# Kernel optimization log

Hardware: AMD Instinct MI355X
Metric: run time of the kernel (lower is better)

## Reference

```python
import jax, jax.numpy as jnp
import numpy as np

B, T, I, H, TGT = 256, 4096, 8, 32, 8


def setup_inputs() -> dict:
    key = jax.random.key(0)
    ks = jax.random.split(key, 6)
    return {
        "inputs": jax.random.normal(ks[0], (B, T, I), jnp.float32),
        "encode_weights": jax.random.normal(ks[1], (H, I), jnp.float32) * 0.3,   # xavier-ish
        "w_ih": jax.random.normal(ks[2], (3 * H, H), jnp.float32) * 0.1,        # GRU weight_ih_l0
        "w_hh": jax.random.normal(ks[3], (3 * H, H), jnp.float32) * 0.1,        # GRU weight_hh_l0
        "b_ih": jax.random.normal(ks[4], (3 * H,), jnp.float32) * 0.1,
        "b_hh": jax.random.normal(ks[5], (3 * H,), jnp.float32) * 0.1,
    }


def _gru(gx_t, w_hh, b_hh, h0):
    # gx_t: time-major input-gate pre-activations [T, B, 3H]; PyTorch GRU math:
    # r = sig(gx_r + gh_r); z = sig(gx_z + gh_z); n = tanh(gx_n + r*gh_n); h = (1-z)*n + z*h
    Hd = h0.shape[-1]
    def step(h, gx):
        gh = h @ w_hh.T + b_hh                      # [B, 3H]
        r = jax.nn.sigmoid(gx[..., :Hd] + gh[..., :Hd])
        z = jax.nn.sigmoid(gx[..., Hd:2 * Hd] + gh[..., Hd:2 * Hd])
        n = jnp.tanh(gx[..., 2 * Hd:] + r * gh[..., 2 * Hd:])
        h_new = (1.0 - z) * n + z * h
        return h_new, h_new
    _, hs = jax.lax.scan(step, h0, gx_t)            # hs: [T, B, H]
    return hs


def reference(inputs, encode_weights, w_ih, w_hh, b_ih, b_hh):
    # encode = F.linear(inputs, encode_weights)
    encode = jnp.einsum('bti,hi->bth', inputs, encode_weights)      # [B, T, H]
    gx = jnp.einsum('bth,gh->btg', encode, w_ih) + b_ih             # [B, T, 3H]
    gx_t = jnp.swapaxes(gx, 0, 1)                                   # [T, B, 3H]
    h0 = jnp.zeros((inputs.shape[0], encode_weights.shape[0]), inputs.dtype)
    latents = jnp.swapaxes(_gru(gx_t, w_hh, b_hh, h0), 0, 1)        # [B, T, H]
    # tied decoder: F.linear(latents, encode_weights[:, :target_size].T)
    outputs = jnp.einsum('bth,ho->bto', latents, encode_weights[:, :TGT])
    return outputs, latents
```

## Files before the change

### kernel.cpp

```cpp
#include <hip/hip_runtime.h>
#include <hip/hip_bf16.h>
#include <cstdint>
#include <cstddef>

#define Bsz  256
#define Tn   4096
#define In   8
#define Hn   32
#define Gn   96
#define TGTn 8
#define CH   256

__device__ __forceinline__ float rcpf(float x) { return __builtin_amdgcn_rcpf(x); }
__device__ __forceinline__ float sigm(float x) { return rcpf(1.f + __expf(-x)); }
__device__ __forceinline__ float tanhfast(float x) {
    float e = __expf(2.f * x);
    return 1.f - 2.f * rcpf(e + 1.f);
}

__global__ void fuse_wih_kernel(const float* __restrict__ w_ih,
                                const float* __restrict__ E,
                                float* __restrict__ Wf) {
    int tid = threadIdx.x;
    int g = tid >> 3, i = tid & 7;
    float acc = 0.f;
#pragma unroll
    for (int k = 0; k < Hn; ++k)
        acc = fmaf(w_ih[g * Hn + k], E[k * In + i], acc);
    Wf[g * In + i] = acc;
}

__launch_bounds__(64, 1)
__global__ void gru_kernel(const float* __restrict__ x,
                           const float* __restrict__ Wf,
                           const float* __restrict__ w_hh,
                           const float* __restrict__ b_ih,
                           const float* __restrict__ b_hh,
                           float* __restrict__ latents) {
    __shared__ __align__(16) float lds_h[Hn];
    __shared__ __align__(16) float lds_x[CH * In];
    __shared__ __align__(16) float lds_lat[CH * Hn];

    const int lane = threadIdx.x;
    const int grp  = lane >> 5;
    const int j    = lane & 31;
    const int b    = blockIdx.x;

    const float* xb  = x + (size_t)b * Tn * In;
    float* latb      = latents + (size_t)b * Tn * Hn;

    float whr[16], whz[16], whn[16];
#pragma unroll
    for (int q = 0; q < 4; ++q) {
        float4 vr = *(const float4*)&w_hh[(0 * Hn + j) * Hn + grp * 16 + q * 4];
        float4 vz = *(const float4*)&w_hh[(1 * Hn + j) * Hn + grp * 16 + q * 4];
        float4 vn = *(const float4*)&w_hh[(2 * Hn + j) * Hn + grp * 16 + q * 4];
        whr[q*4+0] = vr.x; whr[q*4+1] = vr.y; whr[q*4+2] = vr.z; whr[q*4+3] = vr.w;
        whz[q*4+0] = vz.x; whz[q*4+1] = vz.y; whz[q*4+2] = vz.z; whz[q*4+3] = vz.w;
        whn[q*4+0] = vn.x; whn[q*4+1] = vn.y; whn[q*4+2] = vn.z; whn[q*4+3] = vn.w;
    }
    const float4 wxr = *(const float4*)&Wf[(0 * Hn + j) * In + grp * 4];
    const float4 wxz = *(const float4*)&Wf[(1 * Hn + j) * In + grp * 4];
    const float4 wxn = *(const float4*)&Wf[(2 * Hn + j) * In + grp * 4];

    const float br  = b_ih[j]          + b_hh[j];
    const float bz  = b_ih[Hn + j]     + b_hh[Hn + j];
    const float bxn = b_ih[2 * Hn + j];
    const float bhn = b_hh[2 * Hn + j];

    float hj = 0.f;
    float h16[16];
#pragma unroll
    for (int q = 0; q < 16; ++q) h16[q] = 0.f;

    for (int t0 = 0; t0 < Tn; t0 += CH) {
#pragma unroll
        for (int c = 0; c < 8; ++c) {
            int f4 = c * 64 + lane;
            float4 v = *(const float4*)&xb[(size_t)t0 * In + (size_t)f4 * 4];
            *(float4*)&lds_x[f4 * 4] = v;
        }
        __syncthreads();

#pragma unroll 1
        for (int s = 0; s < CH; ++s) {
            float4 xv = *(const float4*)&lds_x[s * In + grp * 4];

            float ar0 = 0.f, ar1 = 0.f, az0 = 0.f, az1 = 0.f, an0 = 0.f, an1 = 0.f;
#pragma unroll
            for (int q = 0; q < 8; ++q) {
                ar0 = fmaf(h16[2*q],   whr[2*q],   ar0);
                ar1 = fmaf(h16[2*q+1], whr[2*q+1], ar1);
                az0 = fmaf(h16[2*q],   whz[2*q],   az0);
                az1 = fmaf(h16[2*q+1], whz[2*q+1], az1);
                an0 = fmaf(h16[2*q],   whn[2*q],   an0);
                an1 = fmaf(h16[2*q+1], whn[2*q+1], an1);
            }
            float ar   = ar0 + ar1;
            float az   = az0 + az1;
            float aghn = an0 + an1;
            ar = fmaf(xv.x, wxr.x, ar); ar = fmaf(xv.y, wxr.y, ar);
            ar = fmaf(xv.z, wxr.z, ar); ar = fmaf(xv.w, wxr.w, ar);
            az = fmaf(xv.x, wxz.x, az); az = fmaf(xv.y, wxz.y, az);
            az = fmaf(xv.z, wxz.z, az); az = fmaf(xv.w, wxz.w, az);
            float agxn = xv.x * wxn.x;
            agxn = fmaf(xv.y, wxn.y, agxn);
            agxn = fmaf(xv.z, wxn.z, agxn);
            agxn = fmaf(xv.w, wxn.w, agxn);

            ar   += __shfl_xor(ar, 32);
            az   += __shfl_xor(az, 32);
            aghn += __shfl_xor(aghn, 32);
            agxn += __shfl_xor(agxn, 32);

            float r = sigm(ar + br);
            float z = sigm(az + bz);
            float n = tanhfast(agxn + bxn + r * (aghn + bhn));
            hj = n + z * (hj - n);

            __syncthreads();
            if (grp == 0) {
                lds_h[j] = hj;
                lds_lat[s * Hn + j] = hj;
            }
            __syncthreads();
#pragma unroll
            for (int q = 0; q < 4; ++q) {
                float4 hv = *(const float4*)&lds_h[grp * 16 + q * 4];
                h16[q*4+0] = hv.x; h16[q*4+1] = hv.y;
                h16[q*4+2] = hv.z; h16[q*4+3] = hv.w;
            }
        }
        __syncthreads();
#pragma unroll
        for (int c = 0; c < 32; ++c) {
            int f4 = c * 64 + lane;
            float4 v = *(const float4*)&lds_lat[f4 * 4];
            *(float4*)&latb[(size_t)t0 * Hn + (size_t)f4 * 4] = v;
        }
    }
}

__global__ void decode_kernel(const float* __restrict__ lat,
                              const float* __restrict__ E,
                              float* __restrict__ out) {
    __shared__ float ldsE[Hn * TGTn];
    int tid = threadIdx.x;
    if (tid < Hn * TGTn) ldsE[tid] = E[tid];
    __syncthreads();
    size_t idx = (size_t)blockIdx.x * 256 + tid;
    int o      = (int)(idx & (TGTn - 1));
    size_t row = idx >> 3;
    const float* lrow = lat + row * Hn;
    float acc = 0.f;
#pragma unroll
    for (int h = 0; h < Hn; ++h)
        acc = fmaf(lrow[h], ldsE[h * TGTn + o], acc);
    out[idx] = acc;
}

extern "C" void kernel_launch(void* const* d_in, const int* in_sizes, int n_in,
                              void* d_out, int out_size, void* d_ws, size_t ws_size,
                              hipStream_t stream) {
    const float* x    = (const float*)d_in[0];
    const float* E    = (const float*)d_in[1];
    const float* w_ih = (const float*)d_in[2];
    const float* w_hh = (const float*)d_in[3];
    const float* b_ih = (const float*)d_in[4];
    const float* b_hh = (const float*)d_in[5];

    float* out = (float*)d_out;
    float* lat = out + (size_t)Bsz * Tn * TGTn;
    float* Wf  = (float*)d_ws;

    fuse_wih_kernel<<<1, 768, 0, stream>>>(w_ih, E, Wf);
    gru_kernel<<<Bsz, 64, 0, stream>>>(x, Wf, w_hh, b_ih, b_hh, lat);
    decode_kernel<<<(Bsz * Tn * TGTn) / 256, 256, 0, stream>>>(lat, E, out);
}
```

Baseline: 1.156 ms.

## Replace LDS hidden-state exchange with DPP/permlane cross-lane gathers and packed FMAs

The recurrent loop no longer passes the hidden state through shared memory with two barriers per step. Each lane now rebuilds its half of h in registers using permlane16/32 swaps and DPP row rotates, with w_hh columns pre-permuted to match the rotated order. The half-wave reductions use permlane32_swap, the matvec uses packed v2f FMAs, and inputs stream through an 8-deep register ring instead of LDS staging. Latents are written straight to global memory each step rather than buffered, which trades coalesced bulk stores for per-step 128-byte stores.

```diff
diff --git a/kernel.cpp b/kernel.cpp
--- a/kernel.cpp
+++ b/kernel.cpp
@@ -7,9 +7,45 @@
 #define Tn   4096
 #define In   8
 #define Hn   32
-#define Gn   96
 #define TGTn 8
-#define CH   256
+
+typedef float v2f __attribute__((ext_vector_type(2)));
+
+__device__ __forceinline__ v2f pk_fma(v2f a, v2f b, v2f c) {
+    return __builtin_elementwise_fma(a, b, c);
+}
+
+template<int N>
+__device__ __forceinline__ float dpp_ror(float x) {
+    int xi = __float_as_int(x);
+    int r = __builtin_amdgcn_update_dpp(xi, xi, 0x120 + N, 0xF, 0xF, false);
+    return __int_as_float(r);
+}
+
+__device__ __forceinline__ float half_sum(float x) {
+    auto r = __builtin_amdgcn_permlane32_swap(__float_as_int(x), __float_as_int(x),
+                                              false, false);
+    return __int_as_float((int)r[0]) + __int_as_float((int)r[1]);
+}
+
+__device__ __forceinline__ void row16_pair(float x, float& a_out, float& b_out) {
+    auto r = __builtin_amdgcn_permlane16_swap(__float_as_int(x), __float_as_int(x),
+                                              false, false);
+    a_out = __int_as_float((int)r[0]);
+    b_out = __int_as_float((int)r[1]);
+}
+
+__device__ __forceinline__ void gather16(float v, v2f H[8]) {
+    v2f G0; G0.x = v;                G0.y = dpp_ror<1>(v);
+    v2f G1; G1.x = dpp_ror<2>(G0.x); G1.y = dpp_ror<2>(G0.y);
+    v2f G2; G2.x = dpp_ror<4>(G0.x); G2.y = dpp_ror<4>(G0.y);
+    v2f G3; G3.x = dpp_ror<4>(G1.x); G3.y = dpp_ror<4>(G1.y);
+    v2f G4; G4.x = dpp_ror<8>(G0.x); G4.y = dpp_ror<8>(G0.y);
+    v2f G5; G5.x = dpp_ror<8>(G1.x); G5.y = dpp_ror<8>(G1.y);
+    v2f G6; G6.x = dpp_ror<8>(G2.x); G6.y = dpp_ror<8>(G2.y);
+    v2f G7; G7.x = dpp_ror<8>(G3.x); G7.y = dpp_ror<8>(G3.y);
+    H[0]=G0; H[1]=G1; H[2]=G2; H[3]=G3; H[4]=G4; H[5]=G5; H[6]=G6; H[7]=G7;
+}
 
 __device__ __forceinline__ float rcpf(float x) { return __builtin_amdgcn_rcpf(x); }
 __device__ __forceinline__ float sigm(float x) { return rcpf(1.f + __expf(-x)); }
@@ -37,106 +73,121 @@
                            const float* __restrict__ b_ih,
                            const float* __restrict__ b_hh,
                            float* __restrict__ latents) {
-    __shared__ __align__(16) float lds_h[Hn];
-    __shared__ __align__(16) float lds_x[CH * In];
-    __shared__ __align__(16) float lds_lat[CH * Hn];
-
-    const int lane = threadIdx.x;
+    const int lane = threadIdx.x & 63;
     const int grp  = lane >> 5;
     const int j    = lane & 31;
+    const int r16  = lane & 15;
     const int b    = blockIdx.x;
 
-    const float* xb  = x + (size_t)b * Tn * In;
-    float* latb      = latents + (size_t)b * Tn * Hn;
-
-    float whr[16], whz[16], whn[16];
-#pragma unroll
-    for (int q = 0; q < 4; ++q) {
-        float4 vr = *(const float4*)&w_hh[(0 * Hn + j) * Hn + grp * 16 + q * 4];
-        float4 vz = *(const float4*)&w_hh[(1 * Hn + j) * Hn + grp * 16 + q * 4];
-        float4 vn = *(const float4*)&w_hh[(2 * Hn + j) * Hn + grp * 16 + q * 4];
-        whr[q*4+0] = vr.x; whr[q*4+1] = vr.y; whr[q*4+2] = vr.z; whr[q*4+3] = vr.w;
-        whz[q*4+0] = vz.x; whz[q*4+1] = vz.y; whz[q*4+2] = vz.z; whz[q*4+3] = vz.w;
-        whn[q*4+0] = vn.x; whn[q*4+1] = vn.y; whn[q*4+2] = vn.z; whn[q*4+3] = vn.w;
-    }
-    const float4 wxr = *(const float4*)&Wf[(0 * Hn + j) * In + grp * 4];
-    const float4 wxz = *(const float4*)&Wf[(1 * Hn + j) * In + grp * 4];
-    const float4 wxn = *(const float4*)&Wf[(2 * Hn + j) * In + grp * 4];
-
-    const float br  = b_ih[j]          + b_hh[j];
-    const float bz  = b_ih[Hn + j]     + b_hh[Hn + j];
-    const float bxn = b_ih[2 * Hn + j];
-    const float bhn = b_hh[2 * Hn + j];
+    int sidx[16];
+    {
+        v2f P[8];
+        gather16((float)r16, P);
+#pragma unroll
+        for (int q = 0; q < 8; ++q) {
+            sidx[2*q]   = (int)P[q].x;
+            sidx[2*q+1] = (int)P[q].y;
+        }
+    }
+    bool pick_a;
+    {
+        float va, vb;
+        row16_pair((float)j, va, vb);
+        pick_a = ((int)va == grp * 16 + r16);
+    }
+
+    v2f whr[8], whz[8], whn[8];
+#pragma unroll
+    for (int q = 0; q < 8; ++q) {
+        const int c0 = grp * 16 + sidx[2*q], c1 = grp * 16 + sidx[2*q+1];
+        whr[q] = v2f{w_hh[(0*Hn + j)*Hn + c0], w_hh[(0*Hn + j)*Hn + c1]};
+        whz[q] = v2f{w_hh[(1*Hn + j)*Hn + c0], w_hh[(1*Hn + j)*Hn + c1]};
+        whn[q] = v2f{w_hh[(2*Hn + j)*Hn + c0], w_hh[(2*Hn + j)*Hn + c1]};
+    }
+    v2f wxr[2], wxz[2], wxn[2];
+#pragma unroll
+    for (int q = 0; q < 2; ++q) {
+        wxr[q] = v2f{Wf[(0*Hn+j)*In + grp*4 + 2*q], Wf[(0*Hn+j)*In + grp*4 + 2*q + 1]};
+        wxz[q] = v2f{Wf[(1*Hn+j)*In + grp*4 + 2*q], Wf[(1*Hn+j)*In + grp*4 + 2*q + 1]};
+        wxn[q] = v2f{Wf[(2*Hn+j)*In + grp*4 + 2*q], Wf[(2*Hn+j)*In + grp*4 + 2*q + 1]};
+    }
+    const float brh  = 0.5f * (b_ih[j]        + b_hh[j]);
+    const float bzh  = 0.5f * (b_ih[Hn + j]   + b_hh[Hn + j]);
+    const float bxnh = 0.5f * b_ih[2*Hn + j];
+    const float bhnh = 0.5f * b_hh[2*Hn + j];
+
+    const float* xb = x + (size_t)b * Tn * In;
+    float* latb     = latents + (size_t)b * Tn * Hn;
 
     float hj = 0.f;
-    float h16[16];
-#pragma unroll
-    for (int q = 0; q < 16; ++q) h16[q] = 0.f;
-
-    for (int t0 = 0; t0 < Tn; t0 += CH) {
-#pragma unroll
-        for (int c = 0; c < 8; ++c) {
-            int f4 = c * 64 + lane;
-            float4 v = *(const float4*)&xb[(size_t)t0 * In + (size_t)f4 * 4];
-            *(float4*)&lds_x[f4 * 4] = v;
-        }
-        __syncthreads();
+    v2f H[8];
+#pragma unroll
+    for (int q = 0; q < 8; ++q) H[q] = v2f{0.f, 0.f};
+
+    float4 xring[8];
+#pragma unroll
+    for (int u = 0; u < 8; ++u)
+        xring[u] = *(const float4*)&xb[(size_t)u * In + grp * 4];
+
+    float axr, axz, cxn;
+    {
+        float4 xq = xring[0];
+        v2f x0 = v2f{xq.x, xq.y}, x1 = v2f{xq.z, xq.w};
+        v2f zr = v2f{0.f, 0.f};
+        v2f a  = pk_fma(x0, wxr[0], pk_fma(x1, wxr[1], zr));
+        axr = a.x + a.y + brh;
+        v2f bb = pk_fma(x0, wxz[0], pk_fma(x1, wxz[1], zr));
+        axz = bb.x + bb.y + bzh;
+        v2f cc = pk_fma(x0, wxn[0], pk_fma(x1, wxn[1], zr));
+        cxn = half_sum(cc.x + cc.y + bxnh);
+    }
 
 #pragma unroll 1
-        for (int s = 0; s < CH; ++s) {
-            float4 xv = *(const float4*)&lds_x[s * In + grp * 4];
-
-            float ar0 = 0.f, ar1 = 0.f, az0 = 0.f, az1 = 0.f, an0 = 0.f, an1 = 0.f;
+    for (int s0 = 0; s0 < Tn; s0 += 8) {
+#pragma unroll
+        for (int u = 0; u < 8; ++u) {
+            const int s = s0 + u;
+
+            v2f ar = v2f{0.f, 0.f}, az = v2f{0.f, 0.f}, an = v2f{0.f, 0.f};
 #pragma unroll
             for (int q = 0; q < 8; ++q) {
-                ar0 = fmaf(h16[2*q],   whr[2*q],   ar0);
-                ar1 = fmaf(h16[2*q+1], whr[2*q+1], ar1);
-                az0 = fmaf(h16[2*q],   whz[2*q],   az0);
-                az1 = fmaf(h16[2*q+1], whz[2*q+1], az1);
-                an0 = fmaf(h16[2*q],   whn[2*q],   an0);
-                an1 = fmaf(h16[2*q+1], whn[2*q+1], an1);
+                ar = pk_fma(H[q], whr[q], ar);
+                az = pk_fma(H[q], whz[q], az);
+                an = pk_fma(H[q], whn[q], an);
             }
-            float ar   = ar0 + ar1;
-            float az   = az0 + az1;
-            float aghn = an0 + an1;
-            ar = fmaf(xv.x, wxr.x, ar); ar = fmaf(xv.y, wxr.y, ar);
-            ar = fmaf(xv.z, wxr.z, ar); ar = fmaf(xv.w, wxr.w, ar);
-            az = fmaf(xv.x, wxz.x, az); az = fmaf(xv.y, wxz.y, az);
-            az = fmaf(xv.z, wxz.z, az); az = fmaf(xv.w, wxz.w, az);
-            float agxn = xv.x * wxn.x;
-            agxn = fmaf(xv.y, wxn.y, agxn);
-            agxn = fmaf(xv.z, wxn.z, agxn);
-            agxn = fmaf(xv.w, wxn.w, agxn);
-
-            ar   += __shfl_xor(ar, 32);
-            az   += __shfl_xor(az, 32);
-            aghn += __shfl_xor(aghn, 32);
-            agxn += __shfl_xor(agxn, 32);
-
-            float r = sigm(ar + br);
-            float z = sigm(az + bz);
-            float n = tanhfast(agxn + bxn + r * (aghn + bhn));
+            float pr  = ar.x + ar.y + axr;
+            float pz  = az.x + az.y + axz;
+            float phn = an.x + an.y + bhnh;
+
+            float cr  = half_sum(pr);
+            float cz  = half_sum(pz);
+            float chn = half_sum(phn);
+
+            float r = sigm(cr);
+            float z = sigm(cz);
+            float n = tanhfast(cxn + r * chn);
             hj = n + z * (hj - n);
 
-            __syncthreads();
-            if (grp == 0) {
-                lds_h[j] = hj;
-                lds_lat[s * Hn + j] = hj;
+            float va, vb;
+            row16_pair(hj, va, vb);
+            float v = pick_a ? va : vb;
+            gather16(v, H);
+
+            latb[(size_t)s * Hn + j] = hj;
+
+            {
+                float4 xq = xring[(u + 1) & 7];
+                v2f x0 = v2f{xq.x, xq.y}, x1 = v2f{xq.z, xq.w};
+                v2f zr = v2f{0.f, 0.f};
+                v2f a  = pk_fma(x0, wxr[0], pk_fma(x1, wxr[1], zr));
+                axr = a.x + a.y + brh;
+                v2f bb = pk_fma(x0, wxz[0], pk_fma(x1, wxz[1], zr));
+                axz = bb.x + bb.y + bzh;
+                v2f cc = pk_fma(x0, wxn[0], pk_fma(x1, wxn[1], zr));
+                cxn = half_sum(cc.x + cc.y + bxnh);
             }
-            __syncthreads();
-#pragma unroll
-            for (int q = 0; q < 4; ++q) {
-                float4 hv = *(const float4*)&lds_h[grp * 16 + q * 4];
-                h16[q*4+0] = hv.x; h16[q*4+1] = hv.y;
-                h16[q*4+2] = hv.z; h16[q*4+3] = hv.w;
-            }
-        }
-        __syncthreads();
-#pragma unroll
-        for (int c = 0; c < 32; ++c) {
-            int f4 = c * 64 + lane;
-            float4 v = *(const float4*)&lds_lat[f4 * 4];
-            *(float4*)&latb[(size_t)t0 * Hn + (size_t)f4 * 4] = v;
+            const int sn = (s + 8) & (Tn - 1);
+            xring[u] = *(const float4*)&xb[(size_t)sn * In + grp * 4];
         }
     }
 }
```

Result: faster. 1.004 ms (-13.1%).

## Restructure GRU step: drop barriers, permlane reduction, exp2-folded gates, register prefetch

Applied to the files above, without the earlier changes.

The recurrent step drops both __syncthreads and the LDS staging of inputs and latents. It relies on the block being a single wave, so LDS ordering within that wave is enough. The cross-half reduction switches from ds-based shuffles to permlane32_swap. The ALPHA/BETA scale factors are folded into the weights and biases so that sigmoid and tanh become one exp2 plus one rcp each. Inputs are prefetched into registers four steps ahead, and latents are stored straight to global memory on every step. The aim is to shorten the serial per-timestep latency chain. The cost is narrow per-step global stores from both halves of the wave, and the correctness of the barrier removal rests on the single-wave assumption.

```diff
diff --git a/kernel.cpp b/kernel.cpp
--- a/kernel.cpp
+++ b/kernel.cpp
@@ -7,15 +7,22 @@
 #define Tn   4096
 #define In   8
 #define Hn   32
-#define Gn   96
 #define TGTn 8
-#define CH   256
-
+
+#define ALPHA (-1.44269504088896341f)
+#define BETA  ( 2.88539008177792682f)
+
+#if __has_builtin(__builtin_amdgcn_exp2f)
+__device__ __forceinline__ float exp2f_fast(float x) { return __builtin_amdgcn_exp2f(x); }
+#else
+__device__ __forceinline__ float exp2f_fast(float x) { return __expf(x * 0.69314718056f); }
+#endif
 __device__ __forceinline__ float rcpf(float x) { return __builtin_amdgcn_rcpf(x); }
-__device__ __forceinline__ float sigm(float x) { return rcpf(1.f + __expf(-x)); }
-__device__ __forceinline__ float tanhfast(float x) {
-    float e = __expf(2.f * x);
-    return 1.f - 2.f * rcpf(e + 1.f);
+
+__device__ __forceinline__ float half_sum(float x) {
+    auto r = __builtin_amdgcn_permlane32_swap(__float_as_int(x), __float_as_int(x),
+                                              false, false);
+    return __int_as_float((int)r[0]) + __int_as_float((int)r[1]);
 }
 
 __global__ void fuse_wih_kernel(const float* __restrict__ w_ih,
@@ -30,7 +37,71 @@
     Wf[g * In + i] = acc;
 }
 
-__launch_bounds__(64, 1)
+#define GRU_STEP(XA, XB, XRA, XRB, DO_REFILL)                                        \
+  {                                                                                  \
+             \
+    float ar = br_h, az = bz_h, anx = bxn_f, anh = bhn_h;                            \
+    ar  = fmaf(XA.x, wxr0, ar);  ar  = fmaf(XA.y, wxr1, ar);                         \
+    ar  = fmaf(XA.z, wxr2, ar);  ar  = fmaf(XA.w, wxr3, ar);                         \
+    ar  = fmaf(XB.x, wxr4, ar);  ar  = fmaf(XB.y, wxr5, ar);                         \
+    ar  = fmaf(XB.z, wxr6, ar);  ar  = fmaf(XB.w, wxr7, ar);                         \
+    az  = fmaf(XA.x, wxz0, az);  az  = fmaf(XA.y, wxz1, az);                         \
+    az  = fmaf(XA.z, wxz2, az);  az  = fmaf(XA.w, wxz3, az);                         \
+    az  = fmaf(XB.x, wxz4, az);  az  = fmaf(XB.y, wxz5, az);                         \
+    az  = fmaf(XB.z, wxz6, az);  az  = fmaf(XB.w, wxz7, az);                         \
+    anx = fmaf(XA.x, wxn0, anx); anx = fmaf(XA.y, wxn1, anx);                        \
+    anx = fmaf(XA.z, wxn2, anx); anx = fmaf(XA.w, wxn3, anx);                        \
+    anx = fmaf(XB.x, wxn4, anx); anx = fmaf(XB.y, wxn5, anx);                        \
+    anx = fmaf(XB.z, wxn6, anx); anx = fmaf(XB.w, wxn7, anx);                        \
+                                                    \
+    ar = fmaf(H0,  wr0,  ar);  az = fmaf(H0,  wz0,  az);  anh = fmaf(H0,  wn0,  anh);\
+    ar = fmaf(H1,  wr1,  ar);  az = fmaf(H1,  wz1,  az);  anh = fmaf(H1,  wn1,  anh);\
+    ar = fmaf(H2,  wr2,  ar);  az = fmaf(H2,  wz2,  az);  anh = fmaf(H2,  wn2,  anh);\
+    ar = fmaf(H3,  wr3,  ar);  az = fmaf(H3,  wz3,  az);  anh = fmaf(H3,  wn3,  anh);\
+    ar = fmaf(H4,  wr4,  ar);  az = fmaf(H4,  wz4,  az);  anh = fmaf(H4,  wn4,  anh);\
+    ar = fmaf(H5,  wr5,  ar);  az = fmaf(H5,  wz5,  az);  anh = fmaf(H5,  wn5,  anh);\
+    ar = fmaf(H6,  wr6,  ar);  az = fmaf(H6,  wz6,  az);  anh = fmaf(H6,  wn6,  anh);\
+    ar = fmaf(H7,  wr7,  ar);  az = fmaf(H7,  wz7,  az);  anh = fmaf(H7,  wn7,  anh);\
+    ar = fmaf(H8,  wr8,  ar);  az = fmaf(H8,  wz8,  az);  anh = fmaf(H8,  wn8,  anh);\
+    ar = fmaf(H9,  wr9,  ar);  az = fmaf(H9,  wz9,  az);  anh = fmaf(H9,  wn9,  anh);\
+    ar = fmaf(H10, wr10, ar);  az = fmaf(H10, wz10, az);  anh = fmaf(H10, wn10, anh);\
+    ar = fmaf(H11, wr11, ar);  az = fmaf(H11, wz11, az);  anh = fmaf(H11, wn11, anh);\
+    ar = fmaf(H12, wr12, ar);  az = fmaf(H12, wz12, az);  anh = fmaf(H12, wn12, anh);\
+    ar = fmaf(H13, wr13, ar);  az = fmaf(H13, wz13, az);  anh = fmaf(H13, wn13, anh);\
+    ar = fmaf(H14, wr14, ar);  az = fmaf(H14, wz14, az);  anh = fmaf(H14, wn14, anh);\
+    ar = fmaf(H15, wr15, ar);  az = fmaf(H15, wz15, az);  anh = fmaf(H15, wn15, anh);\
+    float cr  = half_sum(ar);                           \
+    float cz  = half_sum(az);                                                        \
+    float chn = half_sum(anh);                          \
+    float r = rcpf(1.f + exp2f_fast(cr));                                            \
+    float z = rcpf(1.f + exp2f_fast(cz));                                            \
+    float e = exp2f_fast(__builtin_fmaf(r, chn, anx));                               \
+    float u = rcpf(e + 1.f);                                                         \
+    float n = __builtin_fmaf(-2.f, u, 1.f);                                          \
+    hj = __builtin_fmaf(z, hj - n, n);                                               \
+    lds_h[j] = hj;                               \
+    latb_u[j] = hj;                                                                  \
+    latb_u += Hn;                                               \
+    if (DO_REFILL) {                                                                 \
+        XRA = *(const float4*)refp;                                                  \
+        XRB = *(const float4*)(refp + 4);                                            \
+        refp += In;                                             \
+    }                                                                                \
+               \
+    {                                                                                \
+        float4 q0 = *(const float4*)&lds_h[grp * 16 + 0];                            \
+        float4 q1 = *(const float4*)&lds_h[grp * 16 + 4];                            \
+        float4 q2 = *(const float4*)&lds_h[grp * 16 + 8];                            \
+        float4 q3 = *(const float4*)&lds_h[grp * 16 + 12];                           \
+        H0  = q0.x; H1  = q0.y; H2  = q0.z; H3  = q0.w;                              \
+        H4  = q1.x; H5  = q1.y; H6  = q1.z; H7  = q1.w;                              \
+        H8  = q2.x; H9  = q2.y; H10 = q2.z; H11 = q2.w;                              \
+        H12 = q3.x; H13 = q3.y; H14 = q3.z; H15 = q3.w;                              \
+    }                                                                                \
+  }
+
+#define KEEP(v) asm volatile("" : "+v"(v))
+__attribute__((amdgpu_flat_work_group_size(64, 64), amdgpu_waves_per_eu(1, 1)))
 __global__ void gru_kernel(const float* __restrict__ x,
                            const float* __restrict__ Wf,
                            const float* __restrict__ w_hh,
@@ -38,108 +109,70 @@
                            const float* __restrict__ b_hh,
                            float* __restrict__ latents) {
     __shared__ __align__(16) float lds_h[Hn];
-    __shared__ __align__(16) float lds_x[CH * In];
-    __shared__ __align__(16) float lds_lat[CH * Hn];
-
-    const int lane = threadIdx.x;
+
+    const int lane = threadIdx.x & 63;
     const int grp  = lane >> 5;
     const int j    = lane & 31;
     const int b    = blockIdx.x;
 
-    const float* xb  = x + (size_t)b * Tn * In;
-    float* latb      = latents + (size_t)b * Tn * Hn;
-
-    float whr[16], whz[16], whn[16];
-#pragma unroll
-    for (int q = 0; q < 4; ++q) {
-        float4 vr = *(const float4*)&w_hh[(0 * Hn + j) * Hn + grp * 16 + q * 4];
-        float4 vz = *(const float4*)&w_hh[(1 * Hn + j) * Hn + grp * 16 + q * 4];
-        float4 vn = *(const float4*)&w_hh[(2 * Hn + j) * Hn + grp * 16 + q * 4];
-        whr[q*4+0] = vr.x; whr[q*4+1] = vr.y; whr[q*4+2] = vr.z; whr[q*4+3] = vr.w;
-        whz[q*4+0] = vz.x; whz[q*4+1] = vz.y; whz[q*4+2] = vz.z; whz[q*4+3] = vz.w;
-        whn[q*4+0] = vn.x; whn[q*4+1] = vn.y; whn[q*4+2] = vn.z; whn[q*4+3] = vn.w;
+    float wr0,wr1,wr2,wr3,wr4,wr5,wr6,wr7,wr8,wr9,wr10,wr11,wr12,wr13,wr14,wr15;
+    float wz0,wz1,wz2,wz3,wz4,wz5,wz6,wz7,wz8,wz9,wz10,wz11,wz12,wz13,wz14,wz15;
+    float wn0,wn1,wn2,wn3,wn4,wn5,wn6,wn7,wn8,wn9,wn10,wn11,wn12,wn13,wn14,wn15;
+#define LOADW(M)                                                                  \
+    {                                                                             \
+        const int c = grp * 16 + M;                                               \
+        wr##M = ALPHA * w_hh[(0*Hn + j)*Hn + c];                                  \
+        wz##M = ALPHA * w_hh[(1*Hn + j)*Hn + c];                                  \
+        wn##M = BETA  * w_hh[(2*Hn + j)*Hn + c];                                  \
+        KEEP(wr##M); KEEP(wz##M); KEEP(wn##M);                                    \
     }
-    const float4 wxr = *(const float4*)&Wf[(0 * Hn + j) * In + grp * 4];
-    const float4 wxz = *(const float4*)&Wf[(1 * Hn + j) * In + grp * 4];
-    const float4 wxn = *(const float4*)&Wf[(2 * Hn + j) * In + grp * 4];
-
-    const float br  = b_ih[j]          + b_hh[j];
-    const float bz  = b_ih[Hn + j]     + b_hh[Hn + j];
-    const float bxn = b_ih[2 * Hn + j];
-    const float bhn = b_hh[2 * Hn + j];
+    LOADW(0) LOADW(1) LOADW(2)  LOADW(3)  LOADW(4)  LOADW(5)  LOADW(6)  LOADW(7)
+    LOADW(8) LOADW(9) LOADW(10) LOADW(11) LOADW(12) LOADW(13) LOADW(14) LOADW(15)
+#undef LOADW
+
+    float wxr0,wxr1,wxr2,wxr3,wxr4,wxr5,wxr6,wxr7;
+    float wxz0,wxz1,wxz2,wxz3,wxz4,wxz5,wxz6,wxz7;
+    float wxn0,wxn1,wxn2,wxn3,wxn4,wxn5,wxn6,wxn7;
+#define LOADX(I)                                                                  \
+    wxr##I = 0.5f * ALPHA * Wf[(0*Hn + j)*In + I];                                \
+    wxz##I = 0.5f * ALPHA * Wf[(1*Hn + j)*In + I];                                \
+    wxn##I = BETA         * Wf[(2*Hn + j)*In + I];                                \
+    KEEP(wxr##I); KEEP(wxz##I); KEEP(wxn##I);
+    LOADX(0) LOADX(1) LOADX(2) LOADX(3) LOADX(4) LOADX(5) LOADX(6) LOADX(7)
+#undef LOADX
+
+    float br_h  = 0.5f * ALPHA * (b_ih[j]        + b_hh[j]);
+    float bz_h  = 0.5f * ALPHA * (b_ih[Hn + j]   + b_hh[Hn + j]);
+    float bxn_f = BETA * b_ih[2*Hn + j];
+    float bhn_h = 0.5f * BETA * b_hh[2*Hn + j];
+    KEEP(br_h); KEEP(bz_h); KEEP(bxn_f); KEEP(bhn_h);
+
+    const float* xb   = x + (size_t)b * Tn * In;
+    float* latb_u     = latents + (size_t)b * Tn * Hn;
+    const float* refp = xb + 4 * In;
 
     float hj = 0.f;
-    float h16[16];
-#pragma unroll
-    for (int q = 0; q < 16; ++q) h16[q] = 0.f;
-
-    for (int t0 = 0; t0 < Tn; t0 += CH) {
-#pragma unroll
-        for (int c = 0; c < 8; ++c) {
-            int f4 = c * 64 + lane;
-            float4 v = *(const float4*)&xb[(size_t)t0 * In + (size_t)f4 * 4];
-            *(float4*)&lds_x[f4 * 4] = v;
-        }
-        __syncthreads();
+    float H0=0.f,H1=0.f,H2=0.f,H3=0.f,H4=0.f,H5=0.f,H6=0.f,H7=0.f,
+          H8=0.f,H9=0.f,H10=0.f,H11=0.f,H12=0.f,H13=0.f,H14=0.f,H15=0.f;
+
+    float4 a0 = *(const float4*)&xb[0*In], b0 = *(const float4*)&xb[0*In + 4];
+    float4 a1 = *(const float4*)&xb[1*In], b1 = *(const float4*)&xb[1*In + 4];
+    float4 a2 = *(const float4*)&xb[2*In], b2 = *(const float4*)&xb[2*In + 4];
+    float4 a3 = *(const float4*)&xb[3*In], b3 = *(const float4*)&xb[3*In + 4];
 
 #pragma unroll 1
-        for (int s = 0; s < CH; ++s) {
-            float4 xv = *(const float4*)&lds_x[s * In + grp * 4];
-
-            float ar0 = 0.f, ar1 = 0.f, az0 = 0.f, az1 = 0.f, an0 = 0.f, an1 = 0.f;
-#pragma unroll
-            for (int q = 0; q < 8; ++q) {
-                ar0 = fmaf(h16[2*q],   whr[2*q],   ar0);
-                ar1 = fmaf(h16[2*q+1], whr[2*q+1], ar1);
-                az0 = fmaf(h16[2*q],   whz[2*q],   az0);
-                az1 = fmaf(h16[2*q+1], whz[2*q+1], az1);
-                an0 = fmaf(h16[2*q],   whn[2*q],   an0);
-                an1 = fmaf(h16[2*q+1], whn[2*q+1], an1);
-            }
-            float ar   = ar0 + ar1;
-            float az   = az0 + az1;
-            float aghn = an0 + an1;
-            ar = fmaf(xv.x, wxr.x, ar); ar = fmaf(xv.y, wxr.y, ar);
-            ar = fmaf(xv.z, wxr.z, ar); ar = fmaf(xv.w, wxr.w, ar);
-            az = fmaf(xv.x, wxz.x, az); az = fmaf(xv.y, wxz.y, az);
-            az = fmaf(xv.z, wxz.z, az); az = fmaf(xv.w, wxz.w, az);
-            float agxn = xv.x * wxn.x;
-            agxn = fmaf(xv.y, wxn.y, agxn);
-            agxn = fmaf(xv.z, wxn.z, agxn);
-            agxn = fmaf(xv.w, wxn.w, agxn);
-
-            ar   += __shfl_xor(ar, 32);
-            az   += __shfl_xor(az, 32);
-            aghn += __shfl_xor(aghn, 32);
-            agxn += __shfl_xor(agxn, 32);
-
-            float r = sigm(ar + br);
-            float z = sigm(az + bz);
-            float n = tanhfast(agxn + bxn + r * (aghn + bhn));
-            hj = n + z * (hj - n);
-
-            __syncthreads();
-            if (grp == 0) {
-                lds_h[j] = hj;
-                lds_lat[s * Hn + j] = hj;
-            }
-            __syncthreads();
-#pragma unroll
-            for (int q = 0; q < 4; ++q) {
-                float4 hv = *(const float4*)&lds_h[grp * 16 + q * 4];
-                h16[q*4+0] = hv.x; h16[q*4+1] = hv.y;
-                h16[q*4+2] = hv.z; h16[q*4+3] = hv.w;
-            }
-        }
-        __syncthreads();
-#pragma unroll
-        for (int c = 0; c < 32; ++c) {
-            int f4 = c * 64 + lane;
-            float4 v = *(const float4*)&lds_lat[f4 * 4];
-            *(float4*)&latb[(size_t)t0 * Hn + (size_t)f4 * 4] = v;
-        }
+    for (int s0 = 0; s0 < Tn - 4; s0 += 4) {
+        GRU_STEP(a0, b0, a0, b0, true)
+        GRU_STEP(a1, b1, a1, b1, true)
+        GRU_STEP(a2, b2, a2, b2, true)
+        GRU_STEP(a3, b3, a3, b3, true)
     }
-}
+    GRU_STEP(a0, b0, a0, b0, false)
+    GRU_STEP(a1, b1, a1, b1, false)
+    GRU_STEP(a2, b2, a2, b2, false)
+    GRU_STEP(a3, b3, a3, b3, false)
+}
+#undef KEEP
 
 __global__ void decode_kernel(const float* __restrict__ lat,
                               const float* __restrict__ E,
```

Measured after the change: 1.143 ms. Within noise of the previous version (-1.1%).
